# Optimization experiments

Hardware: AMD Instinct MI355X
Metric: run time of the kernel (lower is better)

Reference implementation:

```python
import jax, jax.numpy as jnp
import numpy as np

B, N, F_IN, D, K, INTER = 64, 512, 128, 128, 32, 256
EPS = 1e-5


def _bn(x, g, b, axes):
    # BatchNorm in training mode (biased batch statistics), matching torch BN forward
    m = x.mean(axis=axes, keepdims=True)
    v = x.var(axis=axes, keepdims=True)
    return (x - m) * jax.lax.rsqrt(v + EPS) * g + b


def setup_inputs() -> dict:
    key = jax.random.key(0)
    ks = jax.random.split(key, 12)
    u = lambda k, s: jax.random.uniform(k, s, jnp.float32, -0.3, 0.3)
    return {
        "data": jax.random.normal(ks[0], (B, N, F_IN), jnp.float32),
        "emb_weight": u(ks[1], (N, D)),          # nn.Embedding(node_num, dim), kaiming-uniform-ish
        "lin_W": u(ks[2], (F_IN, D)),            # GraphLayer lin (no bias)
        "att_i": u(ks[3], (D,)),
        "att_j": u(ks[4], (D,)),
        "att_em_i": u(ks[5], (D,)),
        "att_em_j": u(ks[6], (D,)),
        "gnn_bias": jnp.zeros((D,), jnp.float32),
        "gnn_bn_g": jnp.ones((D,), jnp.float32),
        "gnn_bn_b": jnp.zeros((D,), jnp.float32),
        "bn_out_g": jnp.ones((D,), jnp.float32),
        "bn_out_b": jnp.zeros((D,), jnp.float32),
        "W1": u(ks[7], (D, INTER)), "b1": jnp.zeros((INTER,), jnp.float32),
        "bn1_g": jnp.ones((INTER,), jnp.float32), "bn1_b": jnp.zeros((INTER,), jnp.float32),
        "W2": u(ks[8], (INTER, INTER)), "b2": jnp.zeros((INTER,), jnp.float32),
        "bn2_g": jnp.ones((INTER,), jnp.float32), "bn2_b": jnp.zeros((INTER,), jnp.float32),
        "W3": u(ks[9], (INTER, 1)), "b3": jnp.zeros((1,), jnp.float32),
    }


def reference(data, emb_weight, lin_W, att_i, att_j, att_em_i, att_em_j,
              gnn_bias, gnn_bn_g, gnn_bn_b, bn_out_g, bn_out_b,
              W1, b1, bn1_g, bn1_b, W2, b2, bn2_g, bn2_b, W3, b3):
    M = B * N
    x = data.reshape(M, F_IN)

    # --- learned graph: cosine similarity + topk over DETACHED embeddings ---
    w = jax.lax.stop_gradient(emb_weight)
    nrm = jnp.linalg.norm(w, axis=-1)
    cos = (w @ w.T) / (nrm[:, None] * nrm[None, :])
    topk_idx = jax.lax.top_k(cos, K)[1]                    # [N, K]

    # gated_edge_index = (j=topk neighbor as source, i as target), tiled per batch
    src0 = topk_idx.reshape(-1)                            # [N*K] sources (j)
    dst0 = jnp.repeat(jnp.arange(N), K)                    # [N*K] targets (i)
    off = (jnp.arange(B) * N)[:, None]
    src = (src0[None, :] + off).reshape(-1)                # [B*N*K]
    dst = (dst0[None, :] + off).reshape(-1)
    valid = src != dst                                     # remove_self_loops
    loops = jnp.arange(M)                                  # add_self_loops
    src = jnp.concatenate([src, loops])
    dst = jnp.concatenate([dst, loops])
    valid = jnp.concatenate([valid, jnp.ones((M,), bool)])

    # --- GraphLayer (GAT-style, heads=1, concat=False) ---
    x_lin = x @ lin_W                                      # [M, D]
    emb_b = jnp.tile(emb_weight, (B, 1))                   # [M, D] embedding repeated per batch
    # per-node score halves; gather scalars at edges instead of [E, 2D] keys
    s_i = x_lin @ att_i + emb_b @ att_em_i                 # key_i . cat(att_i, att_em_i)
    s_j = x_lin @ att_j + emb_b @ att_em_j
    logit = jax.nn.leaky_relu(s_i[dst] + s_j[src], 0.2)    # [E]
    logit = jnp.where(valid, logit, -1e9)                  # removed self-edges contribute 0
    mx = jax.ops.segment_max(logit, dst, num_segments=M)
    e = jnp.where(valid, jnp.exp(logit - mx[dst]), 0.0)
    den = jax.ops.segment_sum(e, dst, num_segments=M)
    alpha = e / den[dst]                                   # softmax over incoming edges
    agg = jax.ops.segment_sum(x_lin[src] * alpha[:, None], dst, num_segments=M)
    gcn = jax.nn.relu(_bn(agg + gnn_bias, gnn_bn_g, gnn_bn_b, (0,)))  # GNNLayer bn+relu

    # --- gating by embedding, BN over channel dim, OutLayer MLP ---
    h = gcn.reshape(B, N, D) * emb_weight[None]            # [B, N, D]
    h = jax.nn.relu(_bn(h, bn_out_g, bn_out_b, (0, 1)))    # BatchNorm1d over D channels
    # dropout p=0.2 is identity in eval mode
    o = jax.nn.relu(_bn(h @ W1 + b1, bn1_g, bn1_b, (0, 1)))
    o = jax.nn.relu(_bn(o @ W2 + b2, bn2_g, bn2_b, (0, 1)))
    o = (o @ W3 + b3).reshape(B, N)                        # out.view(-1, node_num)
    return o
```

## Files before the change

kernel.cpp:

```cpp
#include <hip/hip_runtime.h>
#include <math.h>

#define M_ROWS 32768
#define NNODES 512
#define KNBR   32
#define EPSBN  1e-5f

typedef __bf16 bf16x8 __attribute__((ext_vector_type(8)));
typedef __bf16 bf16x4 __attribute__((ext_vector_type(4)));
typedef __bf16 bf16x2 __attribute__((ext_vector_type(2)));
typedef float  f32x4  __attribute__((ext_vector_type(4)));

#if defined(__has_builtin)
#if __has_builtin(__builtin_amdgcn_global_load_lds)
#define HAVE_GLL 1
#endif
#endif

__device__ __forceinline__ void async_ld16(void* lds, const void* g){
#ifdef HAVE_GLL
    __builtin_amdgcn_global_load_lds((__attribute__((address_space(1))) void*)(g),
                                     (__attribute__((address_space(3))) void*)(lds),
                                     16, 0, 0);
#else
    *(bf16x8*)lds = *(const bf16x8*)g;
#endif
}

__global__ __launch_bounds__(256) void k1_kernel(
    const float* __restrict__ data, const float* __restrict__ emb,
    const float* __restrict__ lin_W, const float* __restrict__ W1,
    const float* __restrict__ W2,
    const float* __restrict__ att_i, const float* __restrict__ att_j,
    const float* __restrict__ aem_i, const float* __restrict__ aem_j,
    int* __restrict__ topk, float* __restrict__ e_i, float* __restrict__ e_j,
    __bf16* __restrict__ Wp1, __bf16* __restrict__ Wp2,
    float* __restrict__ stats, float* __restrict__ gnnpart,
    __bf16* __restrict__ xlin, float* __restrict__ s_i, float* __restrict__ s_j)
{
    __shared__ __align__(16) char sm[50176];
    int bid = blockIdx.x, tid = threadIdx.x;

    if (bid < 512){
        __bf16 (*As)[136] = (__bf16(*)[136])sm;
        bf16x8* Bp = (bf16x8*)(sm + 17408);
        int lane = tid & 63, wv = tid >> 6;
        int mrow = lane & 15, q = lane >> 4;
        int row0 = bid * 64;

        #pragma unroll
        for (int i = 0; i < 8; ++i){
            int g = tid + i*256;
            int kg = g >> 7, c = g & 127;
            bf16x8 pk;
            #pragma unroll
            for (int j = 0; j < 8; ++j) pk[j] = (__bf16)lin_W[(size_t)(kg*8 + j)*128 + c];
            Bp[g] = pk;
        }
        #pragma unroll
        for (int i = 0; i < 4; ++i){
            int p = tid + i*256;
            int r = p >> 4, c8 = p & 15;
            const float* src = &data[(size_t)(row0 + r)*128 + c8*8];
            float4 a0 = *(const float4*)src;
            float4 a1 = *(const float4*)(src + 4);
            bf16x8 o;
            o[0]=(__bf16)a0.x; o[1]=(__bf16)a0.y; o[2]=(__bf16)a0.z; o[3]=(__bf16)a0.w;
            o[4]=(__bf16)a1.x; o[5]=(__bf16)a1.y; o[6]=(__bf16)a1.z; o[7]=(__bf16)a1.w;
            *(bf16x8*)&As[r][c8*8] = o;
        }
        __syncthreads();

        f32x4 acc[8];
        #pragma unroll
        for (int ct = 0; ct < 8; ++ct) acc[ct] = (f32x4){0.f,0.f,0.f,0.f};
        #pragma unroll
        for (int ks = 0; ks < 4; ++ks){
            bf16x8 a = *(const bf16x8*)&As[wv*16 + mrow][ks*32 + q*8];
            #pragma unroll
            for (int ct = 0; ct < 8; ++ct){
                bf16x8 bb = Bp[(ks*4 + q)*128 + ct*16 + mrow];
                acc[ct] = __builtin_amdgcn_mfma_f32_16x16x32_bf16(a, bb, acc[ct], 0, 0, 0);
            }
        }

        float ai[4] = {0,0,0,0}, aj[4] = {0,0,0,0};
        #pragma unroll
        for (int ct = 0; ct < 8; ++ct){
            int col = ct*16 + mrow;
            float wti = att_i[col], wtj = att_j[col];
            #pragma unroll
            for (int reg = 0; reg < 4; ++reg){
                int row = row0 + wv*16 + q*4 + reg;
                float v = acc[ct][reg];
                xlin[(size_t)row*128 + col] = (__bf16)v;
                ai[reg] += v*wti; aj[reg] += v*wtj;
            }
        }
        #pragma unroll
        for (int mask = 1; mask < 16; mask <<= 1){
            #pragma unroll
            for (int reg = 0; reg < 4; ++reg){
                ai[reg] += __shfl_xor(ai[reg], mask);
                aj[reg] += __shfl_xor(aj[reg], mask);
            }
        }
        if (mrow == 0){
            #pragma unroll
            for (int reg = 0; reg < 4; ++reg){
                int row = row0 + wv*16 + q*4 + reg;
                s_i[row] = ai[reg];
                s_j[row] = aj[reg];
            }
        }
        return;
    }

    if (bid >= 1024){
        if (bid == 1072){
            for (int i = tid; i < 1536; i += 256) stats[i] = 0.f;
            for (int i = tid; i < 16384; i += 256) gnnpart[i] = 0.f;
            return;
        }
        int gidx = (bid - 1024)*256 + tid;
        const float* W; __bf16* o; int lg;
        if (gidx < 4096){ W = W1; o = Wp1; lg = gidx; }
        else            { W = W2; o = Wp2; lg = gidx - 4096; }
        int kg = lg >> 8, c = lg & 255;
        bf16x8 pk;
        #pragma unroll
        for (int j = 0; j < 8; ++j) pk[j] = (__bf16)W[(size_t)(kg*8 + j)*256 + c];
        *(bf16x8*)&o[(size_t)lg*8] = pk;
        return;
    }

    float* wi   = (float*)sm;
    float* sval = (float*)(sm + 512);
    int*   sidx = (int*)(sm + 2560);
    int row = bid - 512;
    if (tid < 128) wi[tid] = emb[row*128 + tid];
    __syncthreads();

    if (tid >= 64 && tid < 128){
        int lane = tid - 64;
        float ai = wi[lane]*aem_i[lane] + wi[lane+64]*aem_i[lane+64];
        float aj = wi[lane]*aem_j[lane] + wi[lane+64]*aem_j[lane+64];
        #pragma unroll
        for (int off = 32; off; off >>= 1){
            ai += __shfl_down(ai, off);
            aj += __shfl_down(aj, off);
        }
        if (lane == 0){ e_i[row] = ai; e_j[row] = aj; }
    }

    float ni = 0.f;
    #pragma unroll 8
    for (int d = 0; d < 128; ++d) ni += wi[d]*wi[d];
    float rni = sqrtf(ni);
    for (int jj = tid; jj < 512; jj += 256){
        const float4* wj4 = (const float4*)(emb + jj*128);
        float dot = 0.f, nj = 0.f;
        #pragma unroll 8
        for (int d4 = 0; d4 < 32; ++d4){
            float4 w = wj4[d4];
            dot += wi[4*d4+0]*w.x + wi[4*d4+1]*w.y + wi[4*d4+2]*w.z + wi[4*d4+3]*w.w;
            nj  += w.x*w.x + w.y*w.y + w.z*w.z + w.w*w.w;
        }
        sval[jj] = dot / (rni * sqrtf(nj));
        sidx[jj] = jj;
    }
    __syncthreads();

    #pragma unroll 1
    for (int k = 2; k <= 512; k <<= 1){
        #pragma unroll 1
        for (int j = k >> 1; j > 0; j >>= 1){
            int i2 = ((tid & ~(j-1)) << 1) | (tid & (j-1));
            int p  = i2 | j;
            float vi = sval[i2], vp = sval[p];
            int   xi = sidx[i2], xp = sidx[p];
            bool i_before_p = (vi > vp) || (vi == vp && xi < xp);
            bool up = ((i2 & k) == 0);
            if (up ? !i_before_p : i_before_p){
                sval[i2] = vp; sval[p] = vi;
                sidx[i2] = xp; sidx[p] = xi;
            }
            __syncthreads();
        }
    }
    if (tid < KNBR) topk[row*KNBR + tid] = sidx[tid];
}

__global__ __launch_bounds__(256) void agg_kernel(const __bf16* __restrict__ xl,
                                                  const float* __restrict__ s_i,
                                                  const float* __restrict__ s_j,
                                                  const float* __restrict__ e_i,
                                                  const float* __restrict__ e_j,
                                                  const int* __restrict__ topk,
                                                  const float2* __restrict__ gnn_bias2,
                                                  __bf16* __restrict__ aggp,
                                                  float* __restrict__ gnnpart){
    int tid = threadIdx.x;
    int wv = tid >> 6, lane = tid & 63;
    int blk = blockIdx.x;
    int xcd = blk & 7, grp = blk >> 3;
    int batch = xcd*8 + (grp >> 7);
    int node  = (grp & 127)*4 + wv;
    int m = batch*512 + node;
    int i = node;

    int src; bool valid;
    if (lane < KNBR){ int j = topk[i*KNBR + lane]; src = batch*512 + j; valid = (j != i); }
    else            { src = m; valid = (lane == KNBR); }
    float l = s_i[m] + e_i[i] + s_j[src] + e_j[src & 511];
    l = (l >= 0.f) ? l : 0.2f*l;
    l = valid ? l : -1e30f;
    float mx = l;
    #pragma unroll
    for (int mask = 1; mask < 64; mask <<= 1) mx = fmaxf(mx, __shfl_xor(mx, mask));
    float e = valid ? __expf(l - mx) : 0.f;
    float den = e;
    #pragma unroll
    for (int mask = 1; mask < 64; mask <<= 1) den += __shfl_xor(den, mask);
    float alpha = e / den;

    float ak[33]; int sk[33];
    #pragma unroll
    for (int k = 0; k < 33; ++k){
        ak[k] = __shfl(alpha, k);
        sk[k] = __shfl(src, k);
    }
    float ax0 = 0.f, ay0 = 0.f, ax1 = 0.f, ay1 = 0.f;
    #pragma unroll
    for (int k = 0; k < 33; ++k){
        bf16x2 v = *(const bf16x2*)&xl[(size_t)sk[k]*128 + lane*2];
        if (k & 1){ ax1 += ak[k]*(float)v[0]; ay1 += ak[k]*(float)v[1]; }
        else      { ax0 += ak[k]*(float)v[0]; ay0 += ak[k]*(float)v[1]; }
    }
    float2 bv = gnn_bias2[lane];
    bf16x2 o;
    o[0] = (__bf16)(ax0 + ax1 + bv.x);
    o[1] = (__bf16)(ay0 + ay1 + bv.y);
    *(bf16x2*)&aggp[(size_t)m*128 + lane*2] = o;

    float r0 = (float)o[0], r1 = (float)o[1];
    __shared__ float rS[4][128], rQ[4][128];
    rS[wv][lane*2]   = r0;    rS[wv][lane*2+1] = r1;
    rQ[wv][lane*2]   = r0*r0; rQ[wv][lane*2+1] = r1*r1;
    __syncthreads();
    if (tid < 128){
        float ts = rS[0][tid] + rS[1][tid] + rS[2][tid] + rS[3][tid];
        float tq = rQ[0][tid] + rQ[1][tid] + rQ[2][tid] + rQ[3][tid];
        float* slice = gnnpart + (blk & 63)*256;
        atomicAdd(&slice[tid],       ts);
        atomicAdd(&slice[128 + tid], tq);
    }
}

__global__ __launch_bounds__(256) void hstats_kernel(const __bf16* __restrict__ agg,
                                                     const float* __restrict__ gnnpart,
                                                     float* __restrict__ gnnstats,
                                                     const float* __restrict__ g,
                                                     const float* __restrict__ bta,
                                                     const float* __restrict__ emb,
                                                     float* __restrict__ hstats){
    __shared__ float gred[256];
    int tid = threadIdx.x;
    {
        float t = 0.f;
        #pragma unroll 8
        for (int s2 = 0; s2 < 64; ++s2) t += gnnpart[s2*256 + tid];
        gred[tid] = t;
        if (blockIdx.x == 0) gnnstats[tid] = t;
    }
    __syncthreads();

    int cg = tid & 31, rs = tid >> 5;
    int c0 = cg*4;
    float sc[4], sh[4];
    #pragma unroll
    for (int j = 0; j < 4; ++j){
        float mean = gred[c0+j] * (1.f/32768.f);
        float var  = gred[128 + c0+j] * (1.f/32768.f) - mean*mean;
        sc[j] = g[c0+j] / sqrtf(var + EPSBN);
        sh[j] = bta[c0+j] - mean*sc[j];
    }
    float s[4] = {0,0,0,0}, qq[4] = {0,0,0,0};
    for (int m = blockIdx.x*8 + rs; m < M_ROWS; m += gridDim.x*8){
        bf16x4 v = *(const bf16x4*)&agg[(size_t)m*128 + c0];
        float4 e = *(const float4*)&emb[(size_t)(m & 511)*128 + c0];
        float f0 = fmaxf((float)v[0]*sc[0] + sh[0], 0.f) * e.x;
        float f1 = fmaxf((float)v[1]*sc[1] + sh[1], 0.f) * e.y;
        float f2 = fmaxf((float)v[2]*sc[2] + sh[2], 0.f) * e.z;
        float f3 = fmaxf((float)v[3]*sc[3] + sh[3], 0.f) * e.w;
        s[0]+=f0; qq[0]+=f0*f0; s[1]+=f1; qq[1]+=f1*f1;
        s[2]+=f2; qq[2]+=f2*f2; s[3]+=f3; qq[3]+=f3*f3;
    }
    __shared__ float rS[8][128], rQ[8][128];
    #pragma unroll
    for (int j = 0; j < 4; ++j){ rS[rs][c0+j] = s[j]; rQ[rs][c0+j] = qq[j]; }
    __syncthreads();
    if (tid < 128){
        float ts = 0.f, tq = 0.f;
        #pragma unroll
        for (int u = 0; u < 8; ++u){ ts += rS[u][tid]; tq += rQ[u][tid]; }
        atomicAdd(&hstats[tid],       ts);
        atomicAdd(&hstats[128 + tid], tq);
    }
}

template<bool GATE>
__global__ __launch_bounds__(256) void gemm2_kernel(
    const __bf16* __restrict__ A, int a_stride, int Ktot,
    const float* __restrict__ st1, const float* __restrict__ g1, const float* __restrict__ b1,
    const float* __restrict__ emb,
    const float* __restrict__ st2, const float* __restrict__ g2, const float* __restrict__ b2,
    const __bf16* __restrict__ Wp, int Ctot,
    const float* __restrict__ bias,
    __bf16* __restrict__ outp,
    float* __restrict__ outstats, int outK)
{
    __shared__ __align__(16) __bf16 As[128][136];
    __shared__ __align__(16) __bf16 Bp[16][128][8];
    __shared__ float nsc1[128], nsh1[128], nsc2[128], nsh2[128];
    __shared__ float statS[128], statQ[128];

    int tid  = threadIdx.x;
    int lane = tid & 63, wv = tid >> 6;
    int mrow = lane & 15, q = lane >> 4;
    int wvr = wv & 1, wvc = wv >> 1;
    int cb0  = blockIdx.y * 128;
    int row0 = blockIdx.x * 128;

    f32x4 acc[4][4];
    #pragma unroll
    for (int rt = 0; rt < 4; ++rt)
        #pragma unroll
        for (int ct = 0; ct < 4; ++ct)
            acc[rt][ct] = (f32x4){0.f,0.f,0.f,0.f};

    for (int kc = 0; kc < Ktot; kc += 128){
        if (tid < 128){
            int f = kc + tid;
            float mean = st1[f] * (1.f/32768.f);
            float var  = st1[Ktot + f] * (1.f/32768.f) - mean*mean;
            float sc   = g1[f] / sqrtf(var + EPSBN);
            nsc1[tid] = sc;
            nsh1[tid] = b1[f] - mean*sc;
            if (GATE){
                float mean2 = st2[tid] * (1.f/32768.f);
                float var2  = st2[128 + tid] * (1.f/32768.f) - mean2*mean2;
                float sc2   = g2[tid] / sqrtf(var2 + EPSBN);
                nsc2[tid] = sc2;
                nsh2[tid] = b2[tid] - mean2*sc2;
            }
        }
        __syncthreads();

        int kg0 = kc >> 3;
        #pragma unroll
        for (int i = 0; i < 8; ++i){
            int p = tid + i*256;
            const __bf16* src = Wp + ((size_t)(kg0 + (p>>7))*Ctot + cb0 + (p&127))*8;
            async_ld16((__bf16*)Bp + (size_t)p*8, src);
        }
        #pragma unroll
        for (int i = 0; i < 8; ++i){
            int p = tid + i*256;
            int r = p >> 4, c8 = p & 15;
            bf16x8 v = *(const bf16x8*)&A[(size_t)(row0 + r)*a_stride + kc + c8*8];
            bf16x8 o;
            if (GATE){
                const float* ep = &emb[(size_t)((row0 + r) & 511)*128 + c8*8];
                float4 e0 = *(const float4*)ep;
                float4 e1 = *(const float4*)(ep + 4);
                float ee[8] = {e0.x,e0.y,e0.z,e0.w,e1.x,e1.y,e1.z,e1.w};
                #pragma unroll
                for (int j = 0; j < 8; ++j){
                    int f = c8*8 + j;
                    float hv = fmaxf((float)v[j]*nsc1[f] + nsh1[f], 0.f) * ee[j];
                    o[j] = (__bf16)fmaxf(hv*nsc2[f] + nsh2[f], 0.f);
                }
            } else {
                #pragma unroll
                for (int j = 0; j < 8; ++j){
                    int f = c8*8 + j;
                    o[j] = (__bf16)fmaxf((float)v[j]*nsc1[f] + nsh1[f], 0.f);
                }
            }
            *(bf16x8*)&As[r][c8*8] = o;
        }
        __syncthreads();

        #pragma unroll
        for (int ks = 0; ks < 4; ++ks){
            bf16x8 a[4];
            #pragma unroll
            for (int rt = 0; rt < 4; ++rt)
                a[rt] = *(const bf16x8*)&As[wvr*64 + rt*16 + mrow][ks*32 + q*8];
            #pragma unroll
            for (int ct = 0; ct < 4; ++ct){
                bf16x8 bb = *(const bf16x8*)&Bp[ks*4 + q][wvc*64 + ct*16 + mrow][0];
                #pragma unroll
                for (int rt = 0; rt < 4; ++rt)
                    acc[rt][ct] = __builtin_amdgcn_mfma_f32_16x16x32_bf16(a[rt], bb, acc[rt][ct], 0, 0, 0);
            }
        }
        __syncthreads();
    }

    if (tid < 128){ statS[tid] = 0.f; statQ[tid] = 0.f; }
    __syncthreads();

    float cs[4] = {0,0,0,0}, cq[4] = {0,0,0,0};
    #pragma unroll
    for (int ct = 0; ct < 4; ++ct){
        int lcol = wvc*64 + ct*16 + mrow;
        int col  = cb0 + lcol;
        float bvv = bias[col];
        #pragma unroll
        for (int rt = 0; rt < 4; ++rt){
            #pragma unroll
            for (int reg = 0; reg < 4; ++reg){
                int row = row0 + wvr*64 + rt*16 + q*4 + reg;
                __bf16 ov = (__bf16)(acc[rt][ct][reg] + bvv);
                outp[(size_t)row*Ctot + col] = ov;
                float fv = (float)ov; cs[ct] += fv; cq[ct] += fv*fv;
            }
        }
    }
    #pragma unroll
    for (int ct = 0; ct < 4; ++ct){
        float s  = cs[ct]; s  += __shfl_xor(s, 16);  s  += __shfl_xor(s, 32);
        float qq = cq[ct]; qq += __shfl_xor(qq, 16); qq += __shfl_xor(qq, 32);
        if (q == 0){
            atomicAdd(&statS[wvc*64 + ct*16 + mrow], s);
            atomicAdd(&statQ[wvc*64 + ct*16 + mrow], qq);
        }
    }
    __syncthreads();
    if (tid < 128){
        atomicAdd(&outstats[cb0 + tid],        statS[tid]);
        atomicAdd(&outstats[outK + cb0 + tid], statQ[tid]);
    }
}

__global__ __launch_bounds__(256) void final_kernel(const __bf16* __restrict__ t2,
                                                    const float* __restrict__ st,
                                                    const float* __restrict__ g,
                                                    const float* __restrict__ bta,
                                                    const float* __restrict__ W3,
                                                    const float* __restrict__ b3,
                                                    float* __restrict__ outp){
    int gid = blockIdx.x*256 + threadIdx.x;
    int wid = gid >> 6, lane = gid & 63;
    int c0 = lane*4;
    bf16x4 v  = *(const bf16x4*)&t2[(size_t)wid*256 + c0];
    float4 w3 = *(const float4*)&W3[c0];
    float4 gg = *(const float4*)&g[c0];
    float4 bb = *(const float4*)&bta[c0];
    float4 sm = *(const float4*)&st[c0];
    float4 sq = *(const float4*)&st[256 + c0];
    float accv = 0.f;
    {
        float mean, var, val;
        mean = sm.x*(1.f/32768.f); var = sq.x*(1.f/32768.f) - mean*mean;
        val = ((float)v[0]-mean)*(gg.x/sqrtf(var+EPSBN)) + bb.x; accv += fmaxf(val,0.f)*w3.x;
        mean = sm.y*(1.f/32768.f); var = sq.y*(1.f/32768.f) - mean*mean;
        val = ((float)v[1]-mean)*(gg.y/sqrtf(var+EPSBN)) + bb.y; accv += fmaxf(val,0.f)*w3.y;
        mean = sm.z*(1.f/32768.f); var = sq.z*(1.f/32768.f) - mean*mean;
        val = ((float)v[2]-mean)*(gg.z/sqrtf(var+EPSBN)) + bb.z; accv += fmaxf(val,0.f)*w3.z;
        mean = sm.w*(1.f/32768.f); var = sq.w*(1.f/32768.f) - mean*mean;
        val = ((float)v[3]-mean)*(gg.w/sqrtf(var+EPSBN)) + bb.w; accv += fmaxf(val,0.f)*w3.w;
    }
    for (int off = 32; off; off >>= 1) accv += __shfl_down(accv, off);
    if (lane == 0) outp[wid] = accv + b3[0];
}

extern "C" void kernel_launch(void* const* d_in, const int* in_sizes, int n_in,
                              void* d_out, int out_size, void* d_ws, size_t ws_size,
                              hipStream_t stream)
{
    (void)in_sizes; (void)n_in; (void)out_size; (void)ws_size;
    const float* data   = (const float*)d_in[0];
    const float* emb    = (const float*)d_in[1];
    const float* lin_W  = (const float*)d_in[2];
    const float* att_i  = (const float*)d_in[3];
    const float* att_j  = (const float*)d_in[4];
    const float* aem_i  = (const float*)d_in[5];
    const float* aem_j  = (const float*)d_in[6];
    const float* gnn_bias = (const float*)d_in[7];
    const float* gnn_g  = (const float*)d_in[8];
    const float* gnn_b  = (const float*)d_in[9];
    const float* bno_g  = (const float*)d_in[10];
    const float* bno_b  = (const float*)d_in[11];
    const float* W1     = (const float*)d_in[12];
    const float* b1     = (const float*)d_in[13];
    const float* bn1_g  = (const float*)d_in[14];
    const float* bn1_b  = (const float*)d_in[15];
    const float* W2     = (const float*)d_in[16];
    const float* b2     = (const float*)d_in[17];
    const float* bn2_g  = (const float*)d_in[18];
    const float* bn2_b  = (const float*)d_in[19];
    const float* W3     = (const float*)d_in[20];
    const float* b3     = (const float*)d_in[21];
    float* outp = (float*)d_out;
    char*  ws   = (char*)d_ws;

    int*    topk     = (int*)ws;
    float*  e_i      = (float*)(ws + 65536);
    float*  e_j      = (float*)(ws + 67584);
    float*  s_i      = (float*)(ws + 69632);
    float*  s_j      = (float*)(ws + 200704);
    float*  stats    = (float*)(ws + 331776);
    float*  gnnstats = stats;
    float*  hstats   = stats + 256;
    float*  bn1stats = stats + 512;
    float*  bn2stats = stats + 1024;
    __bf16* Wp1      = (__bf16*)(ws + 337920);
    __bf16* Wp2      = (__bf16*)(ws + 403456);
    float*  gnnpart  = (float*)(ws + 534528);
    __bf16* xlin     = (__bf16*)(ws + 1048576);
    __bf16* aggb     = (__bf16*)(ws + 1048576 +   8388608);
    __bf16* t1       = (__bf16*)(ws + 1048576 + 2*8388608);
    __bf16* t2       = (__bf16*)(ws + 1048576 + 2*8388608 + 16777216);

    k1_kernel<<<1073, 256, 0, stream>>>(data, emb, lin_W, W1, W2, att_i, att_j,
                                        aem_i, aem_j, topk, e_i, e_j,
                                        Wp1, Wp2, stats, gnnpart, xlin, s_i, s_j);

    agg_kernel<<<8192, 256, 0, stream>>>(xlin, s_i, s_j, e_i, e_j, topk,
                                         (const float2*)gnn_bias, aggb, gnnpart);

    hstats_kernel<<<256, 256, 0, stream>>>(aggb, gnnpart, gnnstats,
                                           gnn_g, gnn_b, emb, hstats);

    gemm2_kernel<true><<<dim3(256,2), 256, 0, stream>>>(
        aggb, 128, 128, gnnstats, gnn_g, gnn_b, emb, hstats, bno_g, bno_b,
        Wp1, 256, b1, t1, bn1stats, 256);

    gemm2_kernel<false><<<dim3(256,2), 256, 0, stream>>>(
        t1, 256, 256, bn1stats, bn1_g, bn1_b, nullptr, nullptr, nullptr, nullptr,
        Wp2, 256, b2, t2, bn2stats, 256);

    final_kernel<<<M_ROWS/4, 256, 0, stream>>>(t2, bn2stats, bn2_g, bn2_b, W3, b3, outp);
}
```

Measured before the change: 240.6 us.

## Fuse final BN+MLP head into second GEMM via grid barrier, drop t2 buffer

The second MLP GEMM keeps its accumulators in registers. It publishes BN2 statistics, then waits on a global atomic counter, acting as a grid-wide barrier across all 512 blocks. After that it applies BN2+ReLU and the W3 dot product directly, accumulating into the output with atomics. This removes the t2 write and read and the separate final kernel launch. The first GEMM is also specialised into a non-templated, single-K-chunk gate kernel. The grid barrier relies on all 512 blocks being co-resident, otherwise it deadlocks. Output summation order now depends on atomic ordering.

```diff
diff --git a/kernel.cpp b/kernel.cpp
--- a/kernel.cpp
+++ b/kernel.cpp
@@ -36,6 +36,7 @@
     int* __restrict__ topk, float* __restrict__ e_i, float* __restrict__ e_j,
     __bf16* __restrict__ Wp1, __bf16* __restrict__ Wp2,
     float* __restrict__ stats, float* __restrict__ gnnpart,
+    unsigned int* __restrict__ cnt, float* __restrict__ outp,
     __bf16* __restrict__ xlin, float* __restrict__ s_i, float* __restrict__ s_j)
 {
     __shared__ __align__(16) char sm[50176];
@@ -120,6 +121,8 @@
         if (bid == 1072){
             for (int i = tid; i < 1536; i += 256) stats[i] = 0.f;
             for (int i = tid; i < 16384; i += 256) gnnpart[i] = 0.f;
+            for (int i = tid; i < M_ROWS; i += 256) outp[i] = 0.f;
+            if (tid == 0) *cnt = 0u;
             return;
         }
         int gidx = (bid - 1024)*256 + tid;
@@ -309,16 +312,15 @@
     }
 }
 
-template<bool GATE>
-__global__ __launch_bounds__(256) void gemm2_kernel(
-    const __bf16* __restrict__ A, int a_stride, int Ktot,
+__global__ __launch_bounds__(256) void gemm_gate_kernel(
+    const __bf16* __restrict__ A,
     const float* __restrict__ st1, const float* __restrict__ g1, const float* __restrict__ b1,
     const float* __restrict__ emb,
     const float* __restrict__ st2, const float* __restrict__ g2, const float* __restrict__ b2,
-    const __bf16* __restrict__ Wp, int Ctot,
+    const __bf16* __restrict__ Wp,
     const float* __restrict__ bias,
     __bf16* __restrict__ outp,
-    float* __restrict__ outstats, int outK)
+    float* __restrict__ outstats)
 {
     __shared__ __align__(16) __bf16 As[128][136];
     __shared__ __align__(16) __bf16 Bp[16][128][8];
@@ -339,75 +341,61 @@
         for (int ct = 0; ct < 4; ++ct)
             acc[rt][ct] = (f32x4){0.f,0.f,0.f,0.f};
 
-    for (int kc = 0; kc < Ktot; kc += 128){
-        if (tid < 128){
-            int f = kc + tid;
-            float mean = st1[f] * (1.f/32768.f);
-            float var  = st1[Ktot + f] * (1.f/32768.f) - mean*mean;
-            float sc   = g1[f] / sqrtf(var + EPSBN);
-            nsc1[tid] = sc;
-            nsh1[tid] = b1[f] - mean*sc;
-            if (GATE){
-                float mean2 = st2[tid] * (1.f/32768.f);
-                float var2  = st2[128 + tid] * (1.f/32768.f) - mean2*mean2;
-                float sc2   = g2[tid] / sqrtf(var2 + EPSBN);
-                nsc2[tid] = sc2;
-                nsh2[tid] = b2[tid] - mean2*sc2;
-            }
-        }
-        __syncthreads();
-
-        int kg0 = kc >> 3;
-        #pragma unroll
-        for (int i = 0; i < 8; ++i){
-            int p = tid + i*256;
-            const __bf16* src = Wp + ((size_t)(kg0 + (p>>7))*Ctot + cb0 + (p&127))*8;
-            async_ld16((__bf16*)Bp + (size_t)p*8, src);
-        }
-        #pragma unroll
-        for (int i = 0; i < 8; ++i){
-            int p = tid + i*256;
-            int r = p >> 4, c8 = p & 15;
-            bf16x8 v = *(const bf16x8*)&A[(size_t)(row0 + r)*a_stride + kc + c8*8];
-            bf16x8 o;
-            if (GATE){
-                const float* ep = &emb[(size_t)((row0 + r) & 511)*128 + c8*8];
-                float4 e0 = *(const float4*)ep;
-                float4 e1 = *(const float4*)(ep + 4);
-                float ee[8] = {e0.x,e0.y,e0.z,e0.w,e1.x,e1.y,e1.z,e1.w};
-                #pragma unroll
-                for (int j = 0; j < 8; ++j){
-                    int f = c8*8 + j;
-                    float hv = fmaxf((float)v[j]*nsc1[f] + nsh1[f], 0.f) * ee[j];
-                    o[j] = (__bf16)fmaxf(hv*nsc2[f] + nsh2[f], 0.f);
-                }
-            } else {
-                #pragma unroll
-                for (int j = 0; j < 8; ++j){
-                    int f = c8*8 + j;
-                    o[j] = (__bf16)fmaxf((float)v[j]*nsc1[f] + nsh1[f], 0.f);
-                }
-            }
-            *(bf16x8*)&As[r][c8*8] = o;
-        }
-        __syncthreads();
-
-        #pragma unroll
-        for (int ks = 0; ks < 4; ++ks){
-            bf16x8 a[4];
+    if (tid < 128){
+        float mean = st1[tid] * (1.f/32768.f);
+        float var  = st1[128 + tid] * (1.f/32768.f) - mean*mean;
+        float sc   = g1[tid] / sqrtf(var + EPSBN);
+        nsc1[tid] = sc;
+        nsh1[tid] = b1[tid] - mean*sc;
+        float mean2 = st2[tid] * (1.f/32768.f);
+        float var2  = st2[128 + tid] * (1.f/32768.f) - mean2*mean2;
+        float sc2   = g2[tid] / sqrtf(var2 + EPSBN);
+        nsc2[tid] = sc2;
+        nsh2[tid] = b2[tid] - mean2*sc2;
+    }
+    __syncthreads();
+
+    #pragma unroll
+    for (int i = 0; i < 8; ++i){
+        int p = tid + i*256;
+        const __bf16* src = Wp + ((size_t)(p>>7)*256 + cb0 + (p&127))*8;
+        async_ld16((__bf16*)Bp + (size_t)p*8, src);
+    }
+    #pragma unroll
+    for (int i = 0; i < 8; ++i){
+        int p = tid + i*256;
+        int r = p >> 4, c8 = p & 15;
+        bf16x8 v = *(const bf16x8*)&A[(size_t)(row0 + r)*128 + c8*8];
+        const float* ep = &emb[(size_t)((row0 + r) & 511)*128 + c8*8];
+        float4 e0 = *(const float4*)ep;
+        float4 e1 = *(const float4*)(ep + 4);
+        float ee[8] = {e0.x,e0.y,e0.z,e0.w,e1.x,e1.y,e1.z,e1.w};
+        bf16x8 o;
+        #pragma unroll
+        for (int j = 0; j < 8; ++j){
+            int f = c8*8 + j;
+            float hv = fmaxf((float)v[j]*nsc1[f] + nsh1[f], 0.f) * ee[j];
+            o[j] = (__bf16)fmaxf(hv*nsc2[f] + nsh2[f], 0.f);
+        }
+        *(bf16x8*)&As[r][c8*8] = o;
+    }
+    __syncthreads();
+
+    #pragma unroll
+    for (int ks = 0; ks < 4; ++ks){
+        bf16x8 a[4];
+        #pragma unroll
+        for (int rt = 0; rt < 4; ++rt)
+            a[rt] = *(const bf16x8*)&As[wvr*64 + rt*16 + mrow][ks*32 + q*8];
+        #pragma unroll
+        for (int ct = 0; ct < 4; ++ct){
+            bf16x8 bb = *(const bf16x8*)&Bp[ks*4 + q][wvc*64 + ct*16 + mrow][0];
             #pragma unroll
             for (int rt = 0; rt < 4; ++rt)
-                a[rt] = *(const bf16x8*)&As[wvr*64 + rt*16 + mrow][ks*32 + q*8];
-            #pragma unroll
-            for (int ct = 0; ct < 4; ++ct){
-                bf16x8 bb = *(const bf16x8*)&Bp[ks*4 + q][wvc*64 + ct*16 + mrow][0];
-                #pragma unroll
-                for (int rt = 0; rt < 4; ++rt)
-                    acc[rt][ct] = __builtin_amdgcn_mfma_f32_16x16x32_bf16(a[rt], bb, acc[rt][ct], 0, 0, 0);
-            }
-        }
-        __syncthreads();
-    }
+                acc[rt][ct] = __builtin_amdgcn_mfma_f32_16x16x32_bf16(a[rt], bb, acc[rt][ct], 0, 0, 0);
+        }
+    }
+    __syncthreads();
 
     if (tid < 128){ statS[tid] = 0.f; statQ[tid] = 0.f; }
     __syncthreads();
@@ -424,7 +412,7 @@
             for (int reg = 0; reg < 4; ++reg){
                 int row = row0 + wvr*64 + rt*16 + q*4 + reg;
                 __bf16 ov = (__bf16)(acc[rt][ct][reg] + bvv);
-                outp[(size_t)row*Ctot + col] = ov;
+                outp[(size_t)row*256 + col] = ov;
                 float fv = (float)ov; cs[ct] += fv; cq[ct] += fv*fv;
             }
         }
@@ -441,40 +429,168 @@
     __syncthreads();
     if (tid < 128){
         atomicAdd(&outstats[cb0 + tid],        statS[tid]);
-        atomicAdd(&outstats[outK + cb0 + tid], statQ[tid]);
+        atomicAdd(&outstats[256 + cb0 + tid],  statQ[tid]);
     }
 }
 
-__global__ __launch_bounds__(256) void final_kernel(const __bf16* __restrict__ t2,
-                                                    const float* __restrict__ st,
-                                                    const float* __restrict__ g,
-                                                    const float* __restrict__ bta,
-                                                    const float* __restrict__ W3,
-                                                    const float* __restrict__ b3,
-                                                    float* __restrict__ outp){
-    int gid = blockIdx.x*256 + threadIdx.x;
-    int wid = gid >> 6, lane = gid & 63;
-    int c0 = lane*4;
-    bf16x4 v  = *(const bf16x4*)&t2[(size_t)wid*256 + c0];
-    float4 w3 = *(const float4*)&W3[c0];
-    float4 gg = *(const float4*)&g[c0];
-    float4 bb = *(const float4*)&bta[c0];
-    float4 sm = *(const float4*)&st[c0];
-    float4 sq = *(const float4*)&st[256 + c0];
-    float accv = 0.f;
-    {
-        float mean, var, val;
-        mean = sm.x*(1.f/32768.f); var = sq.x*(1.f/32768.f) - mean*mean;
-        val = ((float)v[0]-mean)*(gg.x/sqrtf(var+EPSBN)) + bb.x; accv += fmaxf(val,0.f)*w3.x;
-        mean = sm.y*(1.f/32768.f); var = sq.y*(1.f/32768.f) - mean*mean;
-        val = ((float)v[1]-mean)*(gg.y/sqrtf(var+EPSBN)) + bb.y; accv += fmaxf(val,0.f)*w3.y;
-        mean = sm.z*(1.f/32768.f); var = sq.z*(1.f/32768.f) - mean*mean;
-        val = ((float)v[2]-mean)*(gg.z/sqrtf(var+EPSBN)) + bb.z; accv += fmaxf(val,0.f)*w3.z;
-        mean = sm.w*(1.f/32768.f); var = sq.w*(1.f/32768.f) - mean*mean;
-        val = ((float)v[3]-mean)*(gg.w/sqrtf(var+EPSBN)) + bb.w; accv += fmaxf(val,0.f)*w3.w;
-    }
-    for (int off = 32; off; off >>= 1) accv += __shfl_down(accv, off);
-    if (lane == 0) outp[wid] = accv + b3[0];
+__global__ __launch_bounds__(256) void gemm_final_kernel(
+    const __bf16* __restrict__ A,
+    const float* __restrict__ st1,
+    const float* __restrict__ g1, const float* __restrict__ b1,
+    const __bf16* __restrict__ Wp,
+    const float* __restrict__ bias,
+    float* __restrict__ bn2stats,
+    unsigned int* __restrict__ cnt,
+    const float* __restrict__ g2, const float* __restrict__ b2n,
+    const float* __restrict__ W3, const float* __restrict__ b3,
+    float* __restrict__ outp)
+{
+    __shared__ __align__(16) __bf16 As[128][136];
+    __shared__ __align__(16) __bf16 Bp[16][128][8];
+    __shared__ float nsc1[128], nsh1[128];
+    __shared__ float statS[128], statQ[128];
+    __shared__ float w3s[128];
+
+    int tid  = threadIdx.x;
+    int lane = tid & 63, wv = tid >> 6;
+    int mrow = lane & 15, q = lane >> 4;
+    int wvr = wv & 1, wvc = wv >> 1;
+    int cb0  = blockIdx.y * 128;
+    int row0 = blockIdx.x * 128;
+
+    f32x4 acc[4][4];
+    #pragma unroll
+    for (int rt = 0; rt < 4; ++rt)
+        #pragma unroll
+        for (int ct = 0; ct < 4; ++ct)
+            acc[rt][ct] = (f32x4){0.f,0.f,0.f,0.f};
+
+    for (int kc = 0; kc < 256; kc += 128){
+        if (tid < 128){
+            int f = kc + tid;
+            float mean = st1[f] * (1.f/32768.f);
+            float var  = st1[256 + f] * (1.f/32768.f) - mean*mean;
+            float sc   = g1[f] / sqrtf(var + EPSBN);
+            nsc1[tid] = sc;
+            nsh1[tid] = b1[f] - mean*sc;
+        }
+        __syncthreads();
+
+        int kg0 = kc >> 3;
+        #pragma unroll
+        for (int i = 0; i < 8; ++i){
+            int p = tid + i*256;
+            const __bf16* src = Wp + ((size_t)(kg0 + (p>>7))*256 + cb0 + (p&127))*8;
+            async_ld16((__bf16*)Bp + (size_t)p*8, src);
+        }
+        #pragma unroll
+        for (int i = 0; i < 8; ++i){
+            int p = tid + i*256;
+            int r = p >> 4, c8 = p & 15;
+            bf16x8 v = *(const bf16x8*)&A[(size_t)(row0 + r)*256 + kc + c8*8];
+            bf16x8 o;
+            #pragma unroll
+            for (int j = 0; j < 8; ++j){
+                int f = c8*8 + j;
+                o[j] = (__bf16)fmaxf((float)v[j]*nsc1[f] + nsh1[f], 0.f);
+            }
+            *(bf16x8*)&As[r][c8*8] = o;
+        }
+        __syncthreads();
+
+        #pragma unroll
+        for (int ks = 0; ks < 4; ++ks){
+            bf16x8 a[4];
+            #pragma unroll
+            for (int rt = 0; rt < 4; ++rt)
+                a[rt] = *(const bf16x8*)&As[wvr*64 + rt*16 + mrow][ks*32 + q*8];
+            #pragma unroll
+            for (int ct = 0; ct < 4; ++ct){
+                bf16x8 bb = *(const bf16x8*)&Bp[ks*4 + q][wvc*64 + ct*16 + mrow][0];
+                #pragma unroll
+                for (int rt = 0; rt < 4; ++rt)
+                    acc[rt][ct] = __builtin_amdgcn_mfma_f32_16x16x32_bf16(a[rt], bb, acc[rt][ct], 0, 0, 0);
+            }
+        }
+        __syncthreads();
+    }
+
+    if (tid < 128){ statS[tid] = 0.f; statQ[tid] = 0.f; }
+    __syncthreads();
+
+    float cs[4] = {0,0,0,0}, cq[4] = {0,0,0,0};
+    #pragma unroll
+    for (int ct = 0; ct < 4; ++ct){
+        int col = cb0 + wvc*64 + ct*16 + mrow;
+        float bvv = bias[col];
+        #pragma unroll
+        for (int rt = 0; rt < 4; ++rt){
+            #pragma unroll
+            for (int reg = 0; reg < 4; ++reg){
+                float fv = acc[rt][ct][reg] + bvv;
+                acc[rt][ct][reg] = fv;
+                cs[ct] += fv; cq[ct] += fv*fv;
+            }
+        }
+    }
+    #pragma unroll
+    for (int ct = 0; ct < 4; ++ct){
+        float s  = cs[ct]; s  += __shfl_xor(s, 16);  s  += __shfl_xor(s, 32);
+        float qq = cq[ct]; qq += __shfl_xor(qq, 16); qq += __shfl_xor(qq, 32);
+        if (q == 0){
+            atomicAdd(&statS[wvc*64 + ct*16 + mrow], s);
+            atomicAdd(&statQ[wvc*64 + ct*16 + mrow], qq);
+        }
+    }
+    __syncthreads();
+    if (tid < 128){
+        atomicAdd(&bn2stats[cb0 + tid],        statS[tid]);
+        atomicAdd(&bn2stats[256 + cb0 + tid],  statQ[tid]);
+    }
+
+    __threadfence();
+    __syncthreads();
+    if (tid == 0){
+        atomicAdd(cnt, 1u);
+        while (atomicAdd(cnt, 0u) < 512u) __builtin_amdgcn_s_sleep(16);
+    }
+    __syncthreads();
+    __threadfence();
+
+    if (tid < 128){
+        int col = cb0 + tid;
+        float s  = atomicAdd(&bn2stats[col], 0.f);
+        float qq = atomicAdd(&bn2stats[256 + col], 0.f);
+        float mean = s * (1.f/32768.f);
+        float var  = qq * (1.f/32768.f) - mean*mean;
+        float sc   = g2[col] / sqrtf(var + EPSBN);
+        nsc1[tid] = sc;
+        nsh1[tid] = b2n[col] - mean*sc;
+        w3s[tid]  = W3[col];
+    }
+    __syncthreads();
+
+    float b3v = b3[0];
+    bool add_b3 = (blockIdx.y == 0) && (wvc == 0);
+    #pragma unroll
+    for (int rt = 0; rt < 4; ++rt){
+        #pragma unroll
+        for (int reg = 0; reg < 4; ++reg){
+            float s = 0.f;
+            #pragma unroll
+            for (int ct = 0; ct < 4; ++ct){
+                int lcol = wvc*64 + ct*16 + mrow;
+                float v = acc[rt][ct][reg]*nsc1[lcol] + nsh1[lcol];
+                s += fmaxf(v, 0.f) * w3s[lcol];
+            }
+            s += __shfl_xor(s, 1); s += __shfl_xor(s, 2);
+            s += __shfl_xor(s, 4); s += __shfl_xor(s, 8);
+            if (mrow == 0){
+                int row = row0 + wvr*64 + rt*16 + q*4 + reg;
+                atomicAdd(&outp[row], add_b3 ? (s + b3v) : s);
+            }
+        }
+    }
 }
 
 extern "C" void kernel_launch(void* const* d_in, const int* in_sizes, int n_in,
@@ -520,14 +636,15 @@
     __bf16* Wp1      = (__bf16*)(ws + 337920);
     __bf16* Wp2      = (__bf16*)(ws + 403456);
     float*  gnnpart  = (float*)(ws + 534528);
+    unsigned int* cnt = (unsigned int*)(ws + 600064);
     __bf16* xlin     = (__bf16*)(ws + 1048576);
     __bf16* aggb     = (__bf16*)(ws + 1048576 +   8388608);
     __bf16* t1       = (__bf16*)(ws + 1048576 + 2*8388608);
-    __bf16* t2       = (__bf16*)(ws + 1048576 + 2*8388608 + 16777216);
 
     k1_kernel<<<1073, 256, 0, stream>>>(data, emb, lin_W, W1, W2, att_i, att_j,
                                         aem_i, aem_j, topk, e_i, e_j,
-                                        Wp1, Wp2, stats, gnnpart, xlin, s_i, s_j);
+                                        Wp1, Wp2, stats, gnnpart, cnt, outp,
+                                        xlin, s_i, s_j);
 
     agg_kernel<<<8192, 256, 0, stream>>>(xlin, s_i, s_j, e_i, e_j, topk,
                                          (const float2*)gnn_bias, aggb, gnnpart);
@@ -535,13 +652,11 @@
     hstats_kernel<<<256, 256, 0, stream>>>(aggb, gnnpart, gnnstats,
                                            gnn_g, gnn_b, emb, hstats);
 
-    gemm2_kernel<true><<<dim3(256,2), 256, 0, stream>>>(
-        aggb, 128, 128, gnnstats, gnn_g, gnn_b, emb, hstats, bno_g, bno_b,
-        Wp1, 256, b1, t1, bn1stats, 256);
-
-    gemm2_kernel<false><<<dim3(256,2), 256, 0, stream>>>(
-        t1, 256, 256, bn1stats, bn1_g, bn1_b, nullptr, nullptr, nullptr, nullptr,
-        Wp2, 256, b2, t2, bn2stats, 256);
-
-    final_kernel<<<M_ROWS/4, 256, 0, stream>>>(t2, bn2stats, bn2_g, bn2_b, W3, b3, outp);
+    gemm_gate_kernel<<<dim3(256,2), 256, 0, stream>>>(
+        aggb, gnnstats, gnn_g, gnn_b, emb, hstats, bno_g, bno_b,
+        Wp1, b1, t1, bn1stats);
+
+    gemm_final_kernel<<<dim3(256,2), 256, 0, stream>>>(
+        t1, bn1stats, bn1_g, bn1_b, Wp2, b2,
+        bn2stats, cnt, bn2_g, bn2_b, W3, b3, outp);
 }
```

New measurement: 304.0 us. 1.26x slower.
